# Kernel tuning notes

Measured on AMD Instinct MI355X. Metric: run time of the kernel, lower is better.

## Reference

```python
import jax, jax.numpy as jnp
import numpy as np
from jax import lax

STRIDE = (1, 1)
PADDING = (1, 1)


def setup_inputs() -> dict:
    key = jax.random.key(0)
    k1, k2 = jax.random.split(key)
    x = jax.random.normal(k1, (32, 128, 56, 56), dtype=jnp.float32)
    kernels = jax.random.normal(k2, (256, 128, 3, 3), dtype=jnp.float32)
    return {"x": x, "kernels": kernels}


def reference(x, kernels):
    # Equivalent to the python-loop correlation conv: NCHW input, OIHW weight,
    # cross-correlation (no kernel flip), stride/padding per module config.
    out = lax.conv_general_dilated(
        x, kernels,
        window_strides=STRIDE,
        padding=[(PADDING[0], PADDING[0]), (PADDING[1], PADDING[1])],
        dimension_numbers=("NCHW", "OIHW", "NCHW"),
    )
    return out
```

## Files before the change

kernel.cpp:

```cpp
#include <hip/hip_runtime.h>
#include <cstdint>

#define N_IMG 32
#define C_IN 128
#define H_IN 56
#define W_IN 56
#define K_OUT 256
#define HW (H_IN * W_IN)
#define M_TOTAL (N_IMG * HW)
#define XP_H 58
#define XP_W 58
#define XP_PLANE (XP_H * XP_W)
#define XP_ELEMS (N_IMG * XP_PLANE * C_IN)
#define WT_ELEMS (9 * K_OUT * C_IN)

typedef __bf16 bf16x8 __attribute__((ext_vector_type(8)));
typedef float f32x4 __attribute__((ext_vector_type(4)));

__device__ __align__(16) unsigned short g_xp[XP_ELEMS];
__device__ __align__(16) unsigned short g_wt[WT_ELEMS];

static __device__ __forceinline__ unsigned short f2bf(float f) {
    unsigned int u = __builtin_bit_cast(unsigned int, f);
    u += 0x7fffu + ((u >> 16) & 1u);
    return (unsigned short)(u >> 16);
}

static __device__ __forceinline__ void async_copy16(const unsigned short* g, unsigned short* l) {
    auto gp = (const __attribute__((address_space(1))) unsigned int*)g;
    auto lp = (__attribute__((address_space(3))) unsigned int*)l;
    __builtin_amdgcn_global_load_lds(gp, lp, 16, 0, 0);
}

__global__ __launch_bounds__(256) void zero_xp() {
    uint4* p = (uint4*)g_xp;
    int i = blockIdx.x * 256 + threadIdx.x;
    p[i] = uint4{0u, 0u, 0u, 0u};
}

__global__ __launch_bounds__(256) void xpose_x(const float* __restrict__ x) {
    __shared__ float tile[C_IN * 57];
    const int h = blockIdx.x;
    const int n = blockIdx.y;
    const int tid = threadIdx.x;
#pragma unroll
    for (int i = 0; i < 28; i++) {
        int e = i * 256 + tid;
        int c = e / 56;
        int w = e - c * 56;
        tile[c * 57 + w] = x[((n * C_IN + c) * H_IN + h) * W_IN + w];
    }
    __syncthreads();
    unsigned int* outp = (unsigned int*)g_xp;
#pragma unroll
    for (int i = 0; i < 14; i++) {
        int u = i * 256 + tid;
        int w = u >> 6;
        int cp = u & 63;
        float a = tile[(2 * cp) * 57 + w];
        float b = tile[(2 * cp + 1) * 57 + w];
        unsigned int pk = (unsigned int)f2bf(a) | ((unsigned int)f2bf(b) << 16);
        int idx = ((n * XP_H + h + 1) * XP_W + (w + 1)) * C_IN + 2 * cp;
        outp[idx >> 1] = pk;
    }
}

__global__ __launch_bounds__(256) void xpose_w(const float* __restrict__ w) {
    int e = blockIdx.x * 256 + threadIdx.x;
    int rr = e >> 15;
    int rem = e & 32767;
    int k = rem >> 7;
    int c = rem & 127;
    g_wt[e] = f2bf(w[(k * C_IN + c) * 9 + rr]);
}

__global__ __launch_bounds__(256, 4) void conv_main(float* __restrict__ out) {
    __shared__ __align__(16) unsigned short As[128 * 32];
    __shared__ __align__(16) unsigned short Bs[128 * 32];
    const unsigned short* xp = g_xp;
    const unsigned short* wt = g_wt;

    const int tid = threadIdx.x;
    const int m0 = blockIdx.x * 128;
    const int k0 = blockIdx.y * 128;
    const int wave = tid >> 6, lane = tid & 63;
    const int wm = (wave & 1) * 64;
    const int wn = (wave >> 1) * 64;
    const int lr = lane & 15;
    const int lq = lane >> 4;

    int a_base[2], b_base[2];
    unsigned short* a_lds[2];
    unsigned short* b_lds[2];
#pragma unroll
    for (int j = 0; j < 2; j++) {
        int u = j * 256 + tid;
        int ml = u >> 2;
        int cg = u & 3;
        int p = m0 + ml;
        int n = p / HW;
        int rem = p - n * HW;
        int h = rem / W_IN;
        int w = rem - h * W_IN;
        a_base[j] = ((n * XP_H + h) * XP_W + w) * C_IN + cg * 8;
        b_base[j] = (k0 + ml) * C_IN + cg * 8;
        a_lds[j] = As + (j * 256 + wave * 64) * 8;
        b_lds[j] = Bs + (j * 256 + wave * 64) * 8;
    }

    f32x4 acc[4][4];
#pragma unroll
    for (int mi = 0; mi < 4; mi++)
#pragma unroll
        for (int ni = 0; ni < 4; ni++)
            acc[mi][ni] = f32x4{0.f, 0.f, 0.f, 0.f};

#pragma unroll
    for (int rr = 0; rr < 9; rr++) {
        const int rs_off = ((rr / 3) * XP_W + (rr % 3)) * C_IN;
        const int wt_off = rr * (K_OUT * C_IN);
#pragma unroll
        for (int c0 = 0; c0 < 128; c0 += 32) {
            async_copy16(xp + a_base[0] + rs_off + c0, a_lds[0]);
            async_copy16(xp + a_base[1] + rs_off + c0, a_lds[1]);
            async_copy16(wt + wt_off + b_base[0] + c0, b_lds[0]);
            async_copy16(wt + wt_off + b_base[1] + c0, b_lds[1]);
            __syncthreads();
            bf16x8 af[4], bfr[4];
#pragma unroll
            for (int i = 0; i < 4; i++)
                af[i] = *(const bf16x8*)(As + (wm + i * 16 + lr) * 32 + lq * 8);
#pragma unroll
            for (int i = 0; i < 4; i++)
                bfr[i] = *(const bf16x8*)(Bs + (wn + i * 16 + lr) * 32 + lq * 8);
#pragma unroll
            for (int mi = 0; mi < 4; mi++)
#pragma unroll
                for (int ni = 0; ni < 4; ni++)
                    acc[mi][ni] = __builtin_amdgcn_mfma_f32_16x16x32_bf16(
                        af[mi], bfr[ni], acc[mi][ni], 0, 0, 0);
            __syncthreads();
        }
    }

#pragma unroll
    for (int mi = 0; mi < 4; mi++) {
        int p = m0 + wm + mi * 16 + lq * 4;
        int n = p / HW;
        int off = p - n * HW;
#pragma unroll
        for (int ni = 0; ni < 4; ni++) {
            int k = k0 + wn + ni * 16 + lr;
            *(f32x4*)(out + (n * K_OUT + k) * HW + off) = acc[mi][ni];
        }
    }
}

extern "C" void kernel_launch(void* const* d_in, const int* in_sizes, int n_in,
                              void* d_out, int out_size, void* d_ws, size_t ws_size,
                              hipStream_t stream) {
    const float* x = (const float*)d_in[0];
    const float* w = (const float*)d_in[1];
    float* out = (float*)d_out;

    hipLaunchKernelGGL(zero_xp, dim3((XP_ELEMS * 2) / 16 / 256), dim3(256), 0, stream);
    hipLaunchKernelGGL(xpose_x, dim3(H_IN, N_IMG), dim3(256), 0, stream, x);
    hipLaunchKernelGGL(xpose_w, dim3(WT_ELEMS / 256), dim3(256), 0, stream, w);
    hipLaunchKernelGGL(conv_main, dim3(M_TOTAL / 128, K_OUT / 128), dim3(256), 0, stream, out);
}
```

Before: 257.8 us.

## Double-buffer LDS tiles in conv GEMM and fold padding zeroing into transpose

The main conv loop is flattened into 36 stages with two LDS buffers, so the async global-to-LDS loads for the next stage are issued before the MFMAs on the current buffer, and one barrier per stage replaces two. The separate zero_xp kernel is removed; xpose_x now zeroes only the halo border rows and columns of the padded buffer. This saves one launch and a full-buffer write pass. The risks are LDS use rising to 32KB per block, which may limit occupancy at 4 blocks/CU, and the correctness of relying on global_load_lds completing before the single barrier.

```diff
diff --git a/kernel.cpp b/kernel.cpp
--- a/kernel.cpp
+++ b/kernel.cpp
@@ -10,9 +10,9 @@
 #define M_TOTAL (N_IMG * HW)
 #define XP_H 58
 #define XP_W 58
-#define XP_PLANE (XP_H * XP_W)
-#define XP_ELEMS (N_IMG * XP_PLANE * C_IN)
+#define XP_ELEMS (N_IMG * XP_H * XP_W * C_IN)
 #define WT_ELEMS (9 * K_OUT * C_IN)
+#define N_STAGE 36
 
 typedef __bf16 bf16x8 __attribute__((ext_vector_type(8)));
 typedef float f32x4 __attribute__((ext_vector_type(4)));
@@ -32,17 +32,24 @@
     __builtin_amdgcn_global_load_lds(gp, lp, 16, 0, 0);
 }
 
-__global__ __launch_bounds__(256) void zero_xp() {
-    uint4* p = (uint4*)g_xp;
-    int i = blockIdx.x * 256 + threadIdx.x;
-    p[i] = uint4{0u, 0u, 0u, 0u};
-}
-
 __global__ __launch_bounds__(256) void xpose_x(const float* __restrict__ x) {
     __shared__ float tile[C_IN * 57];
     const int h = blockIdx.x;
     const int n = blockIdx.y;
     const int tid = threadIdx.x;
+
+    if (tid < 32) {
+        int col = (tid >> 4) * (XP_W - 1);
+        int q = tid & 15;
+        uint4* dst = (uint4*)(g_xp + ((size_t)(n * XP_H + h + 1) * XP_W + col) * C_IN) + q;
+        *dst = uint4{0u, 0u, 0u, 0u};
+    }
+    if (h == 0 || h == H_IN - 1) {
+        int hp = (h == 0) ? 0 : XP_H - 1;
+        uint4* base = (uint4*)(g_xp + ((size_t)(n * XP_H + hp) * XP_W) * C_IN);
+        for (int q = tid; q < (XP_W * C_IN) / 8; q += 256) base[q] = uint4{0u, 0u, 0u, 0u};
+    }
+
 #pragma unroll
     for (int i = 0; i < 28; i++) {
         int e = i * 256 + tid;
@@ -75,8 +82,8 @@
 }
 
 __global__ __launch_bounds__(256, 4) void conv_main(float* __restrict__ out) {
-    __shared__ __align__(16) unsigned short As[128 * 32];
-    __shared__ __align__(16) unsigned short Bs[128 * 32];
+    __shared__ __align__(16) unsigned short As[2][128 * 32];
+    __shared__ __align__(16) unsigned short Bs[2][128 * 32];
     const unsigned short* xp = g_xp;
     const unsigned short* wt = g_wt;
 
@@ -89,9 +96,7 @@
     const int lr = lane & 15;
     const int lq = lane >> 4;
 
-    int a_base[2], b_base[2];
-    unsigned short* a_lds[2];
-    unsigned short* b_lds[2];
+    int a_base[2], b_base[2], lds_off[2];
 #pragma unroll
     for (int j = 0; j < 2; j++) {
         int u = j * 256 + tid;
@@ -104,9 +109,22 @@
         int w = rem - h * W_IN;
         a_base[j] = ((n * XP_H + h) * XP_W + w) * C_IN + cg * 8;
         b_base[j] = (k0 + ml) * C_IN + cg * 8;
-        a_lds[j] = As + (j * 256 + wave * 64) * 8;
-        b_lds[j] = Bs + (j * 256 + wave * 64) * 8;
+        lds_off[j] = (j * 256 + wave * 64) * 8;
     }
+
+    auto issue = [&](int s, int buf) {
+        int rs = s >> 2;
+        int c0 = (s & 3) << 5;
+        int r = (rs * 11) >> 5;
+        int sc = rs - r * 3;
+        int a_off = (r * XP_W + sc) * C_IN + c0;
+        int b_off = rs * (K_OUT * C_IN) + c0;
+#pragma unroll
+        for (int j = 0; j < 2; j++) {
+            async_copy16(xp + a_base[j] + a_off, &As[buf][0] + lds_off[j]);
+            async_copy16(wt + b_base[j] + b_off, &Bs[buf][0] + lds_off[j]);
+        }
+    };
 
     f32x4 acc[4][4];
 #pragma unroll
@@ -115,32 +133,25 @@
         for (int ni = 0; ni < 4; ni++)
             acc[mi][ni] = f32x4{0.f, 0.f, 0.f, 0.f};
 
+    issue(0, 0);
+#pragma unroll 2
+    for (int s = 0; s < N_STAGE; s++) {
+        const int cb = s & 1;
+        __syncthreads();
+        if (s + 1 < N_STAGE) issue(s + 1, cb ^ 1);
+        bf16x8 af[4], bfr[4];
 #pragma unroll
-    for (int rr = 0; rr < 9; rr++) {
-        const int rs_off = ((rr / 3) * XP_W + (rr % 3)) * C_IN;
-        const int wt_off = rr * (K_OUT * C_IN);
+        for (int i = 0; i < 4; i++)
+            af[i] = *(const bf16x8*)(&As[cb][0] + (wm + i * 16 + lr) * 32 + lq * 8);
 #pragma unroll
-        for (int c0 = 0; c0 < 128; c0 += 32) {
-            async_copy16(xp + a_base[0] + rs_off + c0, a_lds[0]);
-            async_copy16(xp + a_base[1] + rs_off + c0, a_lds[1]);
-            async_copy16(wt + wt_off + b_base[0] + c0, b_lds[0]);
-            async_copy16(wt + wt_off + b_base[1] + c0, b_lds[1]);
-            __syncthreads();
-            bf16x8 af[4], bfr[4];
+        for (int i = 0; i < 4; i++)
+            bfr[i] = *(const bf16x8*)(&Bs[cb][0] + (wn + i * 16 + lr) * 32 + lq * 8);
 #pragma unroll
-            for (int i = 0; i < 4; i++)
-                af[i] = *(const bf16x8*)(As + (wm + i * 16 + lr) * 32 + lq * 8);
+        for (int mi = 0; mi < 4; mi++)
 #pragma unroll
-            for (int i = 0; i < 4; i++)
-                bfr[i] = *(const bf16x8*)(Bs + (wn + i * 16 + lr) * 32 + lq * 8);
-#pragma unroll
-            for (int mi = 0; mi < 4; mi++)
-#pragma unroll
-                for (int ni = 0; ni < 4; ni++)
-                    acc[mi][ni] = __builtin_amdgcn_mfma_f32_16x16x32_bf16(
-                        af[mi], bfr[ni], acc[mi][ni], 0, 0, 0);
-            __syncthreads();
-        }
+            for (int ni = 0; ni < 4; ni++)
+                acc[mi][ni] = __builtin_amdgcn_mfma_f32_16x16x32_bf16(
+                    af[mi], bfr[ni], acc[mi][ni], 0, 0, 0);
     }
 
 #pragma unroll
@@ -163,7 +174,6 @@
     const float* w = (const float*)d_in[1];
     float* out = (float*)d_out;
 
-    hipLaunchKernelGGL(zero_xp, dim3((XP_ELEMS * 2) / 16 / 256), dim3(256), 0, stream);
     hipLaunchKernelGGL(xpose_x, dim3(H_IN, N_IMG), dim3(256), 0, stream, x);
     hipLaunchKernelGGL(xpose_w, dim3(WT_ELEMS / 256), dim3(256), 0, stream, w);
     hipLaunchKernelGGL(conv_main, dim3(M_TOTAL / 128, K_OUT / 128), dim3(256), 0, stream, out);
```

After: 256.0 us. Within noise of the previous version (-0.7%).
